# Performance work log

Measured on AMD Instinct MI355X. Metric: run time of the kernel, lower is better.

## Reference

```python
import jax, jax.numpy as jnp
import numpy as np

N_QUBITS = 12
DIM = 2 ** N_QUBITS
BATCH = 2048


def setup_inputs() -> dict:
    key = jax.random.key(0)
    k1, k2, k3 = jax.random.split(key, 3)
    inputs = jax.random.normal(k1, (BATCH, N_QUBITS), dtype=jnp.float32)
    weight = jax.random.normal(k2, (3 + 2 * N_QUBITS,), dtype=jnp.float32)
    entangle_matrix = jax.random.normal(k3, (DIM, DIM), dtype=jnp.float32)
    return {"inputs": inputs, "weight": weight, "entangle_matrix": entangle_matrix}


def _encode(ry_angles, rz_angles):
    # Encoder: state = prod over qubits of first column of (Rz*Ry) per qubit.
    ry = ry_angles / 2
    rz = rz_angles / 2
    a = jnp.cos(ry) * jnp.exp(-1j * rz)  # entry11 (row bit = 0)
    b = jnp.sin(ry) * jnp.exp(1j * rz)   # entry21 (row bit = 1)
    col2 = jnp.stack([a, b], axis=-1).astype(jnp.complex64)  # [B, n, 2]
    B, n = ry.shape
    v = jnp.ones((B, 1), dtype=jnp.complex64)
    for q in range(n):  # Kronecker fold over qubits (big-endian, matches dec2bin)
        v = (v[:, :, None] * col2[:, q][:, None, :]).reshape(B, -1)
    return v  # [B, 2^n]


def _rot_mat(w):
    # rot_mat: per-qubit Rx(w[q]) @ Rz(w[n+q]), then full Kronecker product.
    n = w.shape[0] // 2
    tx = (w[:n] / 2).astype(jnp.complex64)
    tz = (w[n:] / 2).astype(jnp.complex64)
    c, s = jnp.cos(tx), jnp.sin(tx)
    rx = jnp.stack([jnp.stack([c, -1j * s], -1),
                    jnp.stack([-1j * s, c], -1)], -2)  # [n,2,2]
    ez = jnp.exp(-1j * tz)
    zero = jnp.zeros_like(ez)
    rz = jnp.stack([jnp.stack([ez, zero], -1),
                    jnp.stack([zero, jnp.exp(1j * tz)], -1)], -2)  # [n,2,2]
    mats = jnp.einsum('qij,qjk->qik', rx, rz)
    M = mats[0]
    for q in range(1, n):
        M = jnp.kron(M, mats[q])
    return M  # [2^n, 2^n]


def _ry2(theta):
    a = theta / 2
    c, s = jnp.cos(a), jnp.sin(a)
    return jnp.stack([jnp.stack([c, -s]), jnp.stack([s, c])])  # [2,2] real


def _final_rot(th3):
    # final_rot_mat: Rz-form @ Ry-form @ Rx-form (all ry_mat_list), kron with identity.
    rot = _ry2(th3[2]) @ (_ry2(th3[1]) @ _ry2(th3[0]))
    eye = jnp.eye(DIM // 2, dtype=jnp.complex64)
    return jnp.kron(rot.astype(jnp.complex64), eye)  # [DIM, DIM]


def reference(inputs, weight, entangle_matrix):
    # initial=False branch
    ry_angles = inputs
    rz_angles = jnp.square(inputs)
    v = _encode(ry_angles, rz_angles)                 # [B, DIM] complex64
    E = entangle_matrix.astype(jnp.complex64)
    R = _rot_mat(weight[3:])
    M = E @ R @ E                                     # [DIM, DIM]
    v = v @ M.T                                       # tensordot dims ([-1],[-1])
    F = _final_rot(weight[:3])
    v = v @ F.T
    half = DIM // 2
    # vector[:, half:] = 0 then sum |.|^2  <=>  sum over first half
    return jnp.sum(jnp.square(jnp.abs(v[:, :half])), axis=-1)  # [B] float32
```

## Files before the change

### kernel.cpp

```cpp
#include <hip/hip_runtime.h>
#include <math.h>

#define QDIM 4096
#define NQ 12
#define QBATCH 2048

typedef _Float16 f16x8 __attribute__((ext_vector_type(8)));
typedef float f32x4 __attribute__((ext_vector_type(4)));
typedef int i32x4 __attribute__((ext_vector_type(4)));

__device__ __forceinline__ void gld_lds16(const void* gptr, void* ldsptr) {
    __builtin_amdgcn_global_load_lds(
        (const __attribute__((address_space(1))) void*)gptr,
        (__attribute__((address_space(3))) void*)ldsptr,
        16, 0, 0);
}

__device__ __forceinline__ int q8(float x) {
    float y = fminf(fmaxf(x, -127.f), 127.f);
    return (int)rintf(y);
}
__device__ __forceinline__ int pack4_i8(int a, int b, int c, int d) {
    return (a & 0xFF) | ((b & 0xFF) << 8) | ((c & 0xFF) << 16) | ((d & 0xFF) << 24);
}

__global__ __launch_bounds__(256) void conv_kernel(
    const float* __restrict__ E, const float* __restrict__ wgt,
    _Float16* __restrict__ Eh, signed char* __restrict__ G8)
{
    float th = 0.5f * (wgt[0] + wgt[1] + wgt[2]);
    float c0 = cosf(th), c1 = -sinf(th);
    const float qs = 127.f / 6.f;
    size_t flat = ((size_t)blockIdx.x * 256 + threadIdx.x) * 8;
    size_t n = flat >> 12;
    size_t k = flat & (QDIM - 1);
    const float* p0 = E + n * QDIM + k;
    const float* p1 = p0 + (size_t)QBATCH * QDIM;
    float4 a0 = ((const float4*)p0)[0], a1 = ((const float4*)p0)[1];
    float4 b0 = ((const float4*)p1)[0], b1 = ((const float4*)p1)[1];
    f16x8 h0 = { (_Float16)a0.x, (_Float16)a0.y, (_Float16)a0.z, (_Float16)a0.w,
                 (_Float16)a1.x, (_Float16)a1.y, (_Float16)a1.z, (_Float16)a1.w };
    f16x8 h1 = { (_Float16)b0.x, (_Float16)b0.y, (_Float16)b0.z, (_Float16)b0.w,
                 (_Float16)b1.x, (_Float16)b1.y, (_Float16)b1.z, (_Float16)b1.w };
    *(f16x8*)&Eh[n * QDIM + k] = h0;
    *(f16x8*)&Eh[(n + QBATCH) * QDIM + k] = h1;
    float g[8] = { c0*a0.x + c1*b0.x, c0*a0.y + c1*b0.y, c0*a0.z + c1*b0.z, c0*a0.w + c1*b0.w,
                   c0*a1.x + c1*b1.x, c0*a1.y + c1*b1.y, c0*a1.z + c1*b1.z, c0*a1.w + c1*b1.w };
    int2 gp = { pack4_i8(q8(g[0]*qs), q8(g[1]*qs), q8(g[2]*qs), q8(g[3]*qs)),
                pack4_i8(q8(g[4]*qs), q8(g[5]*qs), q8(g[6]*qs), q8(g[7]*qs)) };
    *(int2*)&G8[n * QDIM + k] = gp;
}

__global__ __launch_bounds__(256) void expand_kernel(
    const float* __restrict__ inputs, _Float16* __restrict__ A1,
    float* __restrict__ out)
{
    __shared__ float ab[NQ][4];
    const int b = blockIdx.x;
    const int tid = threadIdx.x;
    if (tid == 0) out[b] = 0.f;
    if (tid < NQ) {
        float x = inputs[b * NQ + tid];
        float ry = 0.5f * x;
        float rz = 0.5f * x * x;
        float ca = cosf(ry), sa = sinf(ry), cz = cosf(rz), sz = sinf(rz);
        ab[tid][0] = ca * cz;  ab[tid][1] = -ca * sz;
        ab[tid][2] = sa * cz;  ab[tid][3] =  sa * sz;
    }
    __syncthreads();
    float pr0 = 1.f, pi0 = 0.f;
#pragma unroll
    for (int q = 0; q < 8; ++q) {
        int bit = (tid >> (7 - q)) & 1;
        float cr = ab[q][bit * 2 + 0], ci = ab[q][bit * 2 + 1];
        float nr = pr0 * cr - pi0 * ci;
        float ni = pr0 * ci + pi0 * cr;
        pr0 = nr; pi0 = ni;
    }
    f16x8 vr[2], vi[2];
#pragma unroll
    for (int u = 0; u < 16; ++u) {
        float pr = pr0, pi = pi0;
#pragma unroll
        for (int q = 8; q < 12; ++q) {
            int bit = (u >> (11 - q)) & 1;
            float cr = ab[q][bit * 2 + 0], ci = ab[q][bit * 2 + 1];
            float nr = pr * cr - pi * ci;
            float ni = pr * ci + pi * cr;
            pr = nr; pi = ni;
        }
        vr[u >> 3][u & 7] = (_Float16)pr;
        vi[u >> 3][u & 7] = (_Float16)pi;
    }
    const int idx0 = tid * 16;
    *(f16x8*)&A1[(size_t)b * QDIM + idx0] = vr[0];
    *(f16x8*)&A1[(size_t)b * QDIM + idx0 + 8] = vr[1];
    *(f16x8*)&A1[(size_t)(b + QBATCH) * QDIM + idx0] = vi[0];
    *(f16x8*)&A1[(size_t)(b + QBATCH) * QDIM + idx0 + 8] = vi[1];
}

__global__ __launch_bounds__(256) void gemm_f16(
    const _Float16* __restrict__ A, const _Float16* __restrict__ B,
    _Float16* __restrict__ C, int N)
{
    const int K = QDIM;
    __shared__ __attribute__((aligned(16))) _Float16 As[128 * 64];
    __shared__ __attribute__((aligned(16))) _Float16 Bs[128 * 64];

    const int tid  = threadIdx.x;
    const int wave = tid >> 6;
    const int lane = tid & 63;
    const int bn0 = blockIdx.x * 128;
    const int bm0 = blockIdx.y * 128;
    const int wm = (wave >> 1) * 64;
    const int wn = (wave & 1) * 64;
    const int q = lane >> 4;
    const int r = lane & 15;
    const int rx = r & 7;

    f32x4 acc[4][4];
#pragma unroll
    for (int i = 0; i < 4; ++i)
#pragma unroll
        for (int j = 0; j < 4; ++j) acc[i][j] = (f32x4){0.f, 0.f, 0.f, 0.f};

    const _Float16* gA[4];
    const _Float16* gB[4];
    char* lA[4];
    char* lB[4];
#pragma unroll
    for (int n = 0; n < 4; ++n) {
        int c = n * 256 + tid;
        int row = c >> 3;
        int gcol = (c & 7) ^ (row & 7);
        gA[n] = A + (size_t)(bm0 + row) * K + gcol * 8;
        gB[n] = B + (size_t)(bn0 + row) * K + gcol * 8;
        lA[n] = (char*)As + (n * 256 + wave * 64) * 16;
        lB[n] = (char*)Bs + (n * 256 + wave * 64) * 16;
    }

    for (int kk = 0; kk < K; kk += 64) {
#pragma unroll
        for (int n = 0; n < 4; ++n) {
            gld_lds16(gA[n] + kk, lA[n]);
            gld_lds16(gB[n] + kk, lB[n]);
        }
        __syncthreads();

#pragma unroll
        for (int s = 0; s < 2; ++s) {
            f16x8 af[4], bf[4];
#pragma unroll
            for (int i = 0; i < 4; ++i) {
                int row = wm + i * 16 + r;
                af[i] = *(const f16x8*)&As[(row * 8 + ((s * 4 + q) ^ rx)) * 8];
            }
#pragma unroll
            for (int j = 0; j < 4; ++j) {
                int row = wn + j * 16 + r;
                bf[j] = *(const f16x8*)&Bs[(row * 8 + ((s * 4 + q) ^ rx)) * 8];
            }
#pragma unroll
            for (int i = 0; i < 4; ++i)
#pragma unroll
                for (int j = 0; j < 4; ++j)
                    acc[i][j] = __builtin_amdgcn_mfma_f32_16x16x32_f16(af[i], bf[j], acc[i][j], 0, 0, 0);
        }
        __syncthreads();
    }

#pragma unroll
    for (int i = 0; i < 4; ++i) {
        const int crow = bm0 + wm + i * 16 + q * 4;
#pragma unroll
        for (int rr = 0; rr < 4; ++rr)
#pragma unroll
            for (int j = 0; j < 4; ++j)
                C[(size_t)(crow + rr) * N + bn0 + wn + j * 16 + r] = (_Float16)acc[i][j][rr];
    }
}

__global__ __launch_bounds__(256) void butterfly_kernel(
    const _Float16* __restrict__ u1, const float* __restrict__ wgt,
    signed char* __restrict__ A2, float* __restrict__ scaleA)
{
    __shared__ float sRe[4366];
    __shared__ float sIm[4366];
    __shared__ float mats[NQ][8];
    __shared__ float red[8];
    const int blk = blockIdx.x;
    const int tid = threadIdx.x;
    const int ah = tid >> 4;
    const int al = tid & 15;

    if (tid < NQ) {
        float tx = 0.5f * wgt[3 + tid];
        float tz = 0.5f * wgt[15 + tid];
        float c = cosf(tx), s = sinf(tx), cz = cosf(tz), sz = sinf(tz);
        mats[tid][0] =  c * cz;  mats[tid][1] = -c * sz;
        mats[tid][2] =  s * sz;  mats[tid][3] = -s * cz;
        mats[tid][4] = -s * sz;  mats[tid][5] = -s * cz;
        mats[tid][6] =  c * cz;  mats[tid][7] =  c * sz;
    }

    float xr[16], xi[16];
    {
        const _Float16* pRe = u1 + (size_t)blk * QDIM + tid * 16;
        const _Float16* pIm = u1 + (size_t)(blk + QBATCH) * QDIM + tid * 16;
        f16x8 r0 = ((const f16x8*)pRe)[0], r1 = ((const f16x8*)pRe)[1];
        f16x8 i0 = ((const f16x8*)pIm)[0], i1 = ((const f16x8*)pIm)[1];
#pragma unroll
        for (int j = 0; j < 8; ++j) {
            xr[j] = (float)r0[j]; xr[8 + j] = (float)r1[j];
            xi[j] = (float)i0[j]; xi[8 + j] = (float)i1[j];
        }
    }
    __syncthreads();

#define BFLY_STAGE(arrR, arrI, K_, Q_)                                         \
    {                                                                          \
        const float m00r = mats[Q_][0], m00i = mats[Q_][1];                    \
        const float m01r = mats[Q_][2], m01i = mats[Q_][3];                    \
        const float m10r = mats[Q_][4], m10i = mats[Q_][5];                    \
        const float m11r = mats[Q_][6], m11i = mats[Q_][7];                    \
        _Pragma("unroll")                                                      \
        for (int t = 0; t < 8; ++t) {                                          \
            int i0 = ((t >> (K_)) << ((K_) + 1)) | (t & ((1 << (K_)) - 1));    \
            int i1 = i0 | (1 << (K_));                                         \
            float x0r = arrR[i0], x0i = arrI[i0];                              \
            float x1r = arrR[i1], x1i = arrI[i1];                              \
            arrR[i0] = m00r * x0r - m00i * x0i + m01r * x1r - m01i * x1i;      \
            arrI[i0] = m00r * x0i + m00i * x0r + m01r * x1i + m01i * x1r;      \
            arrR[i1] = m10r * x0r - m10i * x0i + m11r * x1r - m11i * x1i;      \
            arrI[i1] = m10r * x0i + m10i * x0r + m11r * x1i + m11i * x1r;      \
        }                                                                      \
    }

#pragma unroll
    for (int p = 0; p < 4; ++p) BFLY_STAGE(xr, xi, p, 11 - p);

#pragma unroll
    for (int c = 0; c < 16; ++c) {
        sRe[273 * ah + 17 * al + c] = xr[c];
        sIm[273 * ah + 17 * al + c] = xi[c];
    }
    __syncthreads();

    float yr[16], yi[16];
#pragma unroll
    for (int b = 0; b < 16; ++b) {
        yr[b] = sRe[273 * ah + 17 * b + al];
        yi[b] = sIm[273 * ah + 17 * b + al];
    }
#pragma unroll
    for (int p = 0; p < 4; ++p) BFLY_STAGE(yr, yi, p, 7 - p);

#pragma unroll
    for (int b = 0; b < 16; ++b) {
        sRe[273 * ah + 17 * b + al] = yr[b];
        sIm[273 * ah + 17 * b + al] = yi[b];
    }
    __syncthreads();

    float zr[16], zi[16];
#pragma unroll
    for (int a = 0; a < 16; ++a) {
        zr[a] = sRe[273 * a + 17 * ah + al];
        zi[a] = sIm[273 * a + 17 * ah + al];
    }
#pragma unroll
    for (int p = 0; p < 4; ++p) BFLY_STAGE(zr, zi, p, 3 - p);

    float mR = 0.f, mI = 0.f;
#pragma unroll
    for (int j = 0; j < 16; ++j) {
        mR = fmaxf(mR, fabsf(zr[j]));
        mI = fmaxf(mI, fabsf(zi[j]));
    }
#pragma unroll
    for (int off = 32; off > 0; off >>= 1) {
        mR = fmaxf(mR, __shfl_xor(mR, off, 64));
        mI = fmaxf(mI, __shfl_xor(mI, off, 64));
    }
    const int wid = tid >> 6;
    if ((tid & 63) == 0) { red[wid] = mR; red[4 + wid] = mI; }
    __syncthreads();
    mR = fmaxf(fmaxf(red[0], red[1]), fmaxf(red[2], red[3]));
    mI = fmaxf(fmaxf(red[4], red[5]), fmaxf(red[6], red[7]));
    mR = fmaxf(mR, 1e-30f);
    mI = fmaxf(mI, 1e-30f);
    if (tid == 0) {
        scaleA[blk] = mR / 127.f;
        scaleA[blk + QBATCH] = mI / 127.f;
    }
    const float invR = 127.f / mR, invI = 127.f / mI;

    signed char* oRe = A2 + (size_t)blk * QDIM + ah * 16 + al;
    signed char* oIm = A2 + (size_t)(blk + QBATCH) * QDIM + ah * 16 + al;
#pragma unroll
    for (int a = 0; a < 16; ++a) {
        oRe[a * 256] = (signed char)q8(zr[a] * invR);
        oIm[a * 256] = (signed char)q8(zi[a] * invI);
    }
#undef BFLY_STAGE
}

__global__ __launch_bounds__(256) void gemm2_i8(
    const signed char* __restrict__ A, const signed char* __restrict__ B,
    const float* __restrict__ scaleA, float* __restrict__ out)
{
    const int K = QDIM;
    __shared__ __attribute__((aligned(16))) signed char As[128 * 128];
    __shared__ __attribute__((aligned(16))) signed char Bs[128 * 128];

    const int tid  = threadIdx.x;
    const int wave = tid >> 6;
    const int lane = tid & 63;
    const int bn0 = blockIdx.x * 128;
    const int bm0 = blockIdx.y * 128;
    const int wm = (wave >> 1) * 64;
    const int wn = (wave & 1) * 64;
    const int q = lane >> 4;
    const int r = lane & 15;
    const int rx = r & 7;

    i32x4 acc[4][4];
#pragma unroll
    for (int i = 0; i < 4; ++i)
#pragma unroll
        for (int j = 0; j < 4; ++j) acc[i][j] = (i32x4){0, 0, 0, 0};

    const signed char* gA[4];
    const signed char* gB[4];
    char* lA[4];
    char* lB[4];
#pragma unroll
    for (int n = 0; n < 4; ++n) {
        int c = n * 256 + tid;
        int row = c >> 3;
        int gcol = (c & 7) ^ (row & 7);
        gA[n] = A + (size_t)(bm0 + row) * K + gcol * 16;
        gB[n] = B + (size_t)(bn0 + row) * K + gcol * 16;
        lA[n] = (char*)As + (n * 256 + wave * 64) * 16;
        lB[n] = (char*)Bs + (n * 256 + wave * 64) * 16;
    }

    for (int kk = 0; kk < K; kk += 128) {
#pragma unroll
        for (int n = 0; n < 4; ++n) {
            gld_lds16(gA[n] + kk, lA[n]);
            gld_lds16(gB[n] + kk, lB[n]);
        }
        __syncthreads();

#pragma unroll
        for (int s = 0; s < 2; ++s) {
            i32x4 af[4], bf[4];
#pragma unroll
            for (int i = 0; i < 4; ++i) {
                int row = wm + i * 16 + r;
                af[i] = *(const i32x4*)&As[row * 128 + (((s * 4 + q) ^ rx) * 16)];
            }
#pragma unroll
            for (int j = 0; j < 4; ++j) {
                int row = wn + j * 16 + r;
                bf[j] = *(const i32x4*)&Bs[row * 128 + (((s * 4 + q) ^ rx) * 16)];
            }
#pragma unroll
            for (int i = 0; i < 4; ++i)
#pragma unroll
                for (int j = 0; j < 4; ++j)
                    acc[i][j] = __builtin_amdgcn_mfma_i32_16x16x64_i8(af[i], bf[j], acc[i][j], 0, 0, 0);
        }
        __syncthreads();
    }

    const float dqG = 6.f / 127.f;
#pragma unroll
    for (int i = 0; i < 4; ++i) {
#pragma unroll
        for (int rr = 0; rr < 4; ++rr) {
            const int row = bm0 + wm + i * 16 + q * 4 + rr;
            const float sc = scaleA[row] * dqG;
            float v = 0.f;
#pragma unroll
            for (int j = 0; j < 4; ++j) {
                float t = sc * (float)acc[i][j][rr];
                v = fmaf(t, t, v);
            }
            v += __shfl_xor(v, 1, 64);
            v += __shfl_xor(v, 2, 64);
            v += __shfl_xor(v, 4, 64);
            v += __shfl_xor(v, 8, 64);
            if (r == 0) atomicAdd(&out[row & (QBATCH - 1)], v);
        }
    }
}

extern "C" void kernel_launch(void* const* d_in, const int* in_sizes, int n_in,
                              void* d_out, int out_size, void* d_ws, size_t ws_size,
                              hipStream_t stream)
{
    const float* inputs = (const float*)d_in[0];
    const float* weight = (const float*)d_in[1];
    const float* E      = (const float*)d_in[2];
    float* out = (float*)d_out;

    char* ws = (char*)d_ws;
    const size_t MB = 1024 * 1024;
    _Float16*    Eh     = (_Float16*)   (ws + 0);
    signed char* G8     = (signed char*)(ws + 32 * MB);
    _Float16*    A1     = (_Float16*)   (ws + 40 * MB);
    _Float16*    u1     = (_Float16*)   (ws + 72 * MB);
    signed char* A2     = (signed char*)(ws + 104 * MB);
    float*       scaleA = (float*)      (ws + 120 * MB);

    conv_kernel<<<(QBATCH * QDIM / 8) / 256, 256, 0, stream>>>(E, weight, Eh, G8);
    expand_kernel<<<QBATCH, 256, 0, stream>>>(inputs, A1, out);
    gemm_f16<<<dim3(QDIM / 128, QDIM / 128), 256, 0, stream>>>(A1, Eh, u1, QDIM);
    butterfly_kernel<<<QBATCH, 256, 0, stream>>>(u1, weight, A2, scaleA);
    gemm2_i8<<<dim3(2048 / 128, QDIM / 128), 256, 0, stream>>>(A2, G8, scaleA, out);
}
```

Measured before the change: 324.9 us.

## Rewrite first fp16 GEMM as 256x256 double-buffered pipelined kernel with 8 waves

Replaces the 128x128 single-buffered fp16 GEMM with a 256x256 tile, 512-thread kernel that double-buffers LDS. It interleaves global-to-LDS staging of the next K-slice with MFMA work on the current one, using explicit vmcnt waits, barriers and setprio. The goals are more reuse per LDS load and hiding global-load latency behind compute. In exchange it needs 128KB of LDS and many more accumulator registers, and the grid shrinks to 256 blocks, which may underfill the GPU's CUs.

```diff
diff --git a/kernel.cpp b/kernel.cpp
--- a/kernel.cpp
+++ b/kernel.cpp
@@ -99,85 +99,138 @@
     *(f16x8*)&A1[(size_t)(b + QBATCH) * QDIM + idx0 + 8] = vi[1];
 }
 
-__global__ __launch_bounds__(256) void gemm_f16(
+#define VMCNT(N_) asm volatile("s_waitcnt vmcnt(" #N_ ")" ::: "memory")
+#define SBAR()                              \
+    do {                                    \
+        asm volatile("" ::: "memory");      \
+        __builtin_amdgcn_s_barrier();       \
+        asm volatile("" ::: "memory");      \
+    } while (0)
+
+__global__ __launch_bounds__(512, 2) void gemm_f16_256(
     const _Float16* __restrict__ A, const _Float16* __restrict__ B,
     _Float16* __restrict__ C, int N)
 {
     const int K = QDIM;
-    __shared__ __attribute__((aligned(16))) _Float16 As[128 * 64];
-    __shared__ __attribute__((aligned(16))) _Float16 Bs[128 * 64];
+    __shared__ __attribute__((aligned(16))) _Float16 As[2][256 * 64];
+    __shared__ __attribute__((aligned(16))) _Float16 Bs[2][256 * 64];
 
     const int tid  = threadIdx.x;
     const int wave = tid >> 6;
     const int lane = tid & 63;
-    const int bn0 = blockIdx.x * 128;
-    const int bm0 = blockIdx.y * 128;
-    const int wm = (wave >> 1) * 64;
-    const int wn = (wave & 1) * 64;
+    const int bm0 = blockIdx.y * 256;
+    const int bn0 = blockIdx.x * 256;
+    const int wm0 = (wave >> 2) * 128;
+    const int wn0 = (wave & 3) * 64;
     const int q = lane >> 4;
     const int r = lane & 15;
     const int rx = r & 7;
 
-    f32x4 acc[4][4];
-#pragma unroll
-    for (int i = 0; i < 4; ++i)
+    f32x4 acc[8][4];
+#pragma unroll
+    for (int i = 0; i < 8; ++i)
 #pragma unroll
         for (int j = 0; j < 4; ++j) acc[i][j] = (f32x4){0.f, 0.f, 0.f, 0.f};
 
-    const _Float16* gA[4];
-    const _Float16* gB[4];
-    char* lA[4];
-    char* lB[4];
-#pragma unroll
-    for (int n = 0; n < 4; ++n) {
-        int c = n * 256 + tid;
-        int row = c >> 3;
-        int gcol = (c & 7) ^ (row & 7);
-        gA[n] = A + (size_t)(bm0 + row) * K + gcol * 8;
-        gB[n] = B + (size_t)(bn0 + row) * K + gcol * 8;
-        lA[n] = (char*)As + (n * 256 + wave * 64) * 16;
-        lB[n] = (char*)Bs + (n * 256 + wave * 64) * 16;
-    }
-
-    for (int kk = 0; kk < K; kk += 64) {
-#pragma unroll
-        for (int n = 0; n < 4; ++n) {
-            gld_lds16(gA[n] + kk, lA[n]);
-            gld_lds16(gB[n] + kk, lB[n]);
-        }
-        __syncthreads();
-
-#pragma unroll
-        for (int s = 0; s < 2; ++s) {
-            f16x8 af[4], bf[4];
-#pragma unroll
-            for (int i = 0; i < 4; ++i) {
-                int row = wm + i * 16 + r;
-                af[i] = *(const f16x8*)&As[(row * 8 + ((s * 4 + q) ^ rx)) * 8];
-            }
-#pragma unroll
-            for (int j = 0; j < 4; ++j) {
-                int row = wn + j * 16 + r;
-                bf[j] = *(const f16x8*)&Bs[(row * 8 + ((s * 4 + q) ^ rx)) * 8];
-            }
-#pragma unroll
-            for (int i = 0; i < 4; ++i)
-#pragma unroll
-                for (int j = 0; j < 4; ++j)
-                    acc[i][j] = __builtin_amdgcn_mfma_f32_16x16x32_f16(af[i], bf[j], acc[i][j], 0, 0, 0);
-        }
-        __syncthreads();
-    }
-
-#pragma unroll
-    for (int i = 0; i < 4; ++i) {
-        const int crow = bm0 + wm + i * 16 + q * 4;
+    const int srow = tid >> 3;
+    const int scol = ((tid & 7) ^ (srow & 7)) * 8;
+    const _Float16* gA = A + (size_t)(bm0 + srow) * K + scol;
+    const _Float16* gB = B + (size_t)(bn0 + srow) * K + scol;
+
+#define STG_A(D, KK, NN) gld_lds16(gA + (size_t)(NN) * 64 * K + (KK), &As[D][(NN) * 4096 + wave * 512])
+#define STG_B(D, KK, NN) gld_lds16(gB + (size_t)(NN) * 64 * K + (KK), &Bs[D][(NN) * 4096 + wave * 512])
+
+#define RD_A4(DST, D, IB)                                                          \
+    _Pragma("unroll")                                                              \
+    for (int ii = 0; ii < 4; ++ii) {                                               \
+        _Pragma("unroll")                                                          \
+        for (int ss = 0; ss < 2; ++ss)                                             \
+            DST[ii][ss] = *(const f16x8*)&As[D][(wm0 + ((IB) + ii) * 16 + r) * 64  \
+                                                + (((ss * 4 + q) ^ rx) * 8)];      \
+    }
+#define RD_B2(DST, D, JB)                                                          \
+    _Pragma("unroll")                                                              \
+    for (int jj = 0; jj < 2; ++jj) {                                               \
+        _Pragma("unroll")                                                          \
+        for (int ss = 0; ss < 2; ++ss)                                             \
+            DST[jj][ss] = *(const f16x8*)&Bs[D][(wn0 + ((JB) + jj) * 16 + r) * 64  \
+                                                + (((ss * 4 + q) ^ rx) * 8)];      \
+    }
+#define MM8(AR, BR, I0, J0)                                                        \
+    _Pragma("unroll")                                                              \
+    for (int ii = 0; ii < 4; ++ii) {                                               \
+        _Pragma("unroll")                                                          \
+        for (int jj = 0; jj < 2; ++jj) {                                           \
+            acc[(I0) + ii][(J0) + jj] = __builtin_amdgcn_mfma_f32_16x16x32_f16(    \
+                AR[ii][0], BR[jj][0], acc[(I0) + ii][(J0) + jj], 0, 0, 0);         \
+            acc[(I0) + ii][(J0) + jj] = __builtin_amdgcn_mfma_f32_16x16x32_f16(    \
+                AR[ii][1], BR[jj][1], acc[(I0) + ii][(J0) + jj], 0, 0, 0);         \
+        }                                                                          \
+    }
+
+    f16x8 a0[4][2], a1[4][2], b0[2][2], b1[2][2];
+
+    STG_B(0, 0, 0); STG_B(0, 0, 1); STG_B(0, 0, 2); STG_B(0, 0, 3);
+    STG_A(0, 0, 0); STG_A(0, 0, 2); STG_A(0, 0, 1); STG_A(0, 0, 3);
+    VMCNT(0);
+    SBAR();
+    RD_A4(a0, 0, 0);
+    RD_B2(b0, 0, 0);
+
+    for (int t = 0; t < 64; ++t) {
+        const int d = t & 1;
+        const int e = d ^ 1;
+        const int kn = ((t + 1) & 63) * 64;
+
+        STG_B(e, kn, 0); STG_B(e, kn, 1);
+        VMCNT(2);
+        RD_B2(b1, d, 2);
+        SBAR();
+        __builtin_amdgcn_s_setprio(1);
+        MM8(a0, b0, 0, 0);
+        __builtin_amdgcn_s_setprio(0);
+        SBAR();
+
+        STG_B(e, kn, 2); STG_B(e, kn, 3);
+        RD_A4(a1, d, 4);
+        SBAR();
+        __builtin_amdgcn_s_setprio(1);
+        MM8(a0, b1, 0, 2);
+        __builtin_amdgcn_s_setprio(0);
+        SBAR();
+
+        STG_A(e, kn, 0); STG_A(e, kn, 2);
+        SBAR();
+        __builtin_amdgcn_s_setprio(1);
+        MM8(a1, b1, 4, 2);
+        __builtin_amdgcn_s_setprio(0);
+        SBAR();
+
+        STG_A(e, kn, 1); STG_A(e, kn, 3);
+        VMCNT(2);
+        SBAR();
+        __builtin_amdgcn_s_setprio(1);
+        MM8(a1, b0, 4, 0);
+        __builtin_amdgcn_s_setprio(0);
+        RD_A4(a0, e, 0);
+        RD_B2(b0, e, 0);
+        SBAR();
+    }
+
+#pragma unroll
+    for (int i = 0; i < 8; ++i) {
+        const int crow = bm0 + wm0 + i * 16 + q * 4;
 #pragma unroll
         for (int rr = 0; rr < 4; ++rr)
 #pragma unroll
             for (int j = 0; j < 4; ++j)
-                C[(size_t)(crow + rr) * N + bn0 + wn + j * 16 + r] = (_Float16)acc[i][j][rr];
-    }
+                C[(size_t)(crow + rr) * N + bn0 + wn0 + j * 16 + r] = (_Float16)acc[i][j][rr];
+    }
+#undef STG_A
+#undef STG_B
+#undef RD_A4
+#undef RD_B2
+#undef MM8
 }
 
 __global__ __launch_bounds__(256) void butterfly_kernel(
@@ -417,7 +470,7 @@
 
     conv_kernel<<<(QBATCH * QDIM / 8) / 256, 256, 0, stream>>>(E, weight, Eh, G8);
     expand_kernel<<<QBATCH, 256, 0, stream>>>(inputs, A1, out);
-    gemm_f16<<<dim3(QDIM / 128, QDIM / 128), 256, 0, stream>>>(A1, Eh, u1, QDIM);
+    gemm_f16_256<<<dim3(QDIM / 256, QDIM / 256), 512, 0, stream>>>(A1, Eh, u1, QDIM);
     butterfly_kernel<<<QBATCH, 256, 0, stream>>>(u1, weight, A2, scaleA);
     gemm2_i8<<<dim3(2048 / 128, QDIM / 128), 256, 0, stream>>>(A2, G8, scaleA, out);
 }
```

Result: no change. 318.6 us (-2.0%).
